# Optimization experiments

Hardware: AMD Instinct MI355X
Metric: run time of the kernel (lower is better)

## Reference

```python
import jax, jax.numpy as jnp
import numpy as np

N = 100000
E = 3200000
D = 128
H = 128
BN_EPS = 1e-5


def setup_inputs() -> dict:
    key = jax.random.key(0)
    ks = jax.random.split(key, 8)
    x = jax.random.normal(ks[0], (N, D), dtype=jnp.float32)
    edge_index = jax.random.randint(ks[1], (2, E), 0, N, dtype=jnp.int64)
    edge_attr = jax.random.normal(ks[2], (E, 1), dtype=jnp.float32)
    # MLP params (Linear stores weight [out,in]; we keep [in,out] for x @ W)
    W1 = jax.random.normal(ks[3], (D, H), dtype=jnp.float32) / np.sqrt(D)
    b1 = jnp.zeros((H,), dtype=jnp.float32)
    W2 = jax.random.normal(ks[4], (H, H), dtype=jnp.float32) / np.sqrt(H)
    b2 = jnp.zeros((H,), dtype=jnp.float32)
    gamma = jnp.ones((H,), dtype=jnp.float32)
    beta = jnp.zeros((H,), dtype=jnp.float32)
    return {"x": x, "edge_index": edge_index, "edge_attr": edge_attr,
            "W1": W1, "b1": b1, "W2": W2, "b2": b2,
            "gamma": gamma, "beta": beta}


def reference(x, edge_index, edge_attr, W1, b1, W2, b2, gamma, beta):
    src, dst = edge_index[0], edge_index[1]
    # GIN aggregation: (1 + eps) * x_i + sum_{j->i} x_j, eps = 0
    agg = jax.ops.segment_sum(x[src], dst, num_segments=N)  # [N, D]
    h = x + agg
    # 2-layer MLP
    h = jax.nn.relu(h @ W1 + b1)
    h = h @ W2 + b2
    # outer ReLU
    h = jax.nn.relu(h)
    # BatchNorm1d (training mode: batch stats, biased variance)
    mean = jnp.mean(h, axis=0)
    var = jnp.mean(jnp.square(h - mean), axis=0)
    h = (h - mean) * jax.lax.rsqrt(var + BN_EPS) * gamma + beta
    return h
```

## Files before the change

### kernel.cpp

```cpp
#include <hip/hip_runtime.h>

#define N_NODES 100000
#define DIM 128
#define NBUCK 391
#define CAP 12288
#define PT_TILE 8192
#define PT_THR 512

typedef unsigned int u32;
typedef unsigned short u16;
typedef __attribute__((ext_vector_type(8))) short bf16x8;
typedef __attribute__((ext_vector_type(4))) float f32x4;

__device__ __forceinline__ float bf16_to_f(u16 v) {
  return __uint_as_float(((u32)v) << 16);
}
__device__ __forceinline__ u16 f_to_bf16(float f) {
  u32 b = __float_as_uint(f);
  b += 0x7fff + ((b >> 16) & 1);
  return (u16)(b >> 16);
}
__device__ __forceinline__ float blo(u32 q) { return __uint_as_float(q << 16); }
__device__ __forceinline__ float bhi(u32 q) {
  return __uint_as_float(q & 0xffff0000u);
}
__device__ __forceinline__ u32 packbf(float lo, float hi) {
  return ((u32)f_to_bf16(hi) << 16) | (u32)f_to_bf16(lo);
}

__global__ __launch_bounds__(256) void prep_kernel(
    const float* __restrict__ x, u16* __restrict__ xb,
    const float* __restrict__ W1, u16* __restrict__ Wt1,
    const float* __restrict__ W2, u16* __restrict__ Wt2,
    const int* __restrict__ ei, int* __restrict__ bcnt, int E_) {
  int blk = blockIdx.x;
  if (blk < 2048) {
    int total = N_NODES * DIM / 4;
    int stride = 2048 * 256;
    for (int i = blk * 256 + threadIdx.x; i < total; i += stride) {
      float4 v = reinterpret_cast<const float4*>(x)[i];
      ushort4 o;
      o.x = f_to_bf16(v.x);
      o.y = f_to_bf16(v.y);
      o.z = f_to_bf16(v.z);
      o.w = f_to_bf16(v.w);
      reinterpret_cast<ushort4*>(xb)[i] = o;
    }
  } else if (blk < 2112) {
    int id = (blk - 2048) * 256 + threadIdx.x;
    Wt1[id] = f_to_bf16(W1[(id & 127) * DIM + (id >> 7)]);
  } else if (blk < 2176) {
    int id = (blk - 2112) * 256 + threadIdx.x;
    Wt2[id] = f_to_bf16(W2[(id & 127) * DIM + (id >> 7)]);
  } else {
    __shared__ int lc[NBUCK];
    for (int i = threadIdx.x; i < NBUCK; i += 256) lc[i] = 0;
    __syncthreads();
    const int* dst = ei + E_;
    int G = 512 * 256;
    int g = (blk - 2176) * 256 + threadIdx.x;
    int n4 = E_ >> 2;
    const int4* d4 = (const int4*)dst;
    for (int i = g; i < n4; i += G) {
      int4 v = d4[i];
      atomicAdd(&lc[((u32)v.x) >> 8], 1);
      atomicAdd(&lc[((u32)v.y) >> 8], 1);
      atomicAdd(&lc[((u32)v.z) >> 8], 1);
      atomicAdd(&lc[((u32)v.w) >> 8], 1);
    }
    for (int e = (n4 << 2) + g; e < E_; e += G)
      atomicAdd(&lc[((u32)dst[e]) >> 8], 1);
    __syncthreads();
    for (int i = threadIdx.x; i < NBUCK; i += 256)
      if (lc[i]) atomicAdd(&bcnt[i], lc[i]);
  }
}

__global__ void bscan_kernel(const int* __restrict__ bcnt,
                             int* __restrict__ boffs, int* __restrict__ gcur) {
  __shared__ int s[256];
  int t = threadIdx.x;
  int v0 = (2 * t < NBUCK) ? bcnt[2 * t] : 0;
  int v1 = (2 * t + 1 < NBUCK) ? bcnt[2 * t + 1] : 0;
  int ts = v0 + v1;
  s[t] = ts;
  __syncthreads();
  for (int o = 1; o < 256; o <<= 1) {
    int u = (t >= o) ? s[t - o] : 0;
    __syncthreads();
    s[t] += u;
    __syncthreads();
  }
  int excl = s[t] - ts;
  if (2 * t <= NBUCK) boffs[2 * t] = excl;
  if (2 * t + 1 <= NBUCK) boffs[2 * t + 1] = excl + v0;
  if (2 * t < NBUCK) gcur[2 * t] = excl;
  if (2 * t + 1 < NBUCK) gcur[2 * t + 1] = excl + v0;
}

__global__ __launch_bounds__(PT_THR) void partition_kernel(
    const int* __restrict__ ei, int* __restrict__ gcur,
    u32* __restrict__ packed, int E_) {
  __shared__ u32 keys[PT_TILE];
  __shared__ u16 bid[PT_TILE];
  __shared__ int lh[NBUCK];
  __shared__ int lpos[NBUCK];
  __shared__ int gpos[NBUCK];
  __shared__ int ss[PT_THR];
  const int t = threadIdx.x;
  const int base = blockIdx.x * PT_TILE;
  const int cnt = min(PT_TILE, E_ - base);

  for (int i = t; i < NBUCK; i += PT_THR) lh[i] = 0;
  __syncthreads();

  u32 pk[16];
  int bb[16];
#pragma unroll
  for (int k = 0; k < 16; ++k) {
    int e = base + k * PT_THR + t;
    if (k * PT_THR + t < cnt) {
      int src = ei[e];
      u32 dst = (u32)ei[E_ + e];
      bb[k] = (int)(dst >> 8);
      pk[k] = (u32)src | ((dst & 255u) << 17);
      atomicAdd(&lh[bb[k]], 1);
    } else {
      bb[k] = -1;
    }
  }
  __syncthreads();

  int v = (t < NBUCK) ? lh[t] : 0;
  ss[t] = v;
  __syncthreads();
  for (int o = 1; o < PT_THR; o <<= 1) {
    int u = (t >= o) ? ss[t - o] : 0;
    __syncthreads();
    ss[t] += u;
    __syncthreads();
  }
  if (t < NBUCK) {
    lpos[t] = ss[t] - v;
    if (v > 0) gpos[t] = atomicAdd(&gcur[t], v);
  }
  __syncthreads();

#pragma unroll
  for (int k = 0; k < 16; ++k) {
    if (bb[k] >= 0) {
      int p = atomicAdd(&lpos[bb[k]], 1);
      keys[p] = pk[k];
      bid[p] = (u16)bb[k];
    }
  }
  __syncthreads();

  for (int i = t; i < cnt; i += PT_THR) {
    int b = bid[i];
    int startb = lpos[b] - lh[b];
    packed[gpos[b] + (i - startb)] = keys[i];
  }
}

__global__ __launch_bounds__(256) void bsort_kernel(u32* __restrict__ packed,
                                                    const int* __restrict__ boffs,
                                                    int* __restrict__ offs,
                                                    int E_) {
  __shared__ u32 sorted_[CAP];
  __shared__ int hist[256], cur[256], ss[256];
  const int b = blockIdx.x, t = threadIdx.x;
  int base = boffs[b];
  int cnt = boffs[b + 1] - base;
  if (cnt > CAP) cnt = CAP;
  hist[t] = 0;
  __syncthreads();
  for (int i = t; i < cnt; i += 256) atomicAdd(&hist[packed[base + i] >> 17], 1);
  __syncthreads();
  int hv = hist[t];
  ss[t] = hv;
  __syncthreads();
  for (int o = 1; o < 256; o <<= 1) {
    int u = (t >= o) ? ss[t - o] : 0;
    __syncthreads();
    ss[t] += u;
    __syncthreads();
  }
  int excl = ss[t] - hv;
  cur[t] = excl;
  __syncthreads();
  for (int i = t; i < cnt; i += 256) {
    u32 v = packed[base + i];
    int p = atomicAdd(&cur[v >> 17], 1);
    sorted_[p] = v & 0x1FFFFu;
  }
  __syncthreads();
  for (int i = t; i < cnt; i += 256) packed[base + i] = sorted_[i];
  int node = b * 256 + t;
  if (node < N_NODES) offs[node] = base + excl;
  if (b == 0 && t == 0) offs[N_NODES] = E_;
}

__global__ __launch_bounds__(256) void gather_bf16_kernel(
    const uint4* __restrict__ xb4, const int* __restrict__ offs,
    const int* __restrict__ csr, uint4* __restrict__ hb4) {
  int n = blockIdx.x * 4 + (threadIdx.x >> 6);
  int lane = threadIdx.x & 63;
  int g = lane >> 4;
  int l = lane & 15;
  int beg = offs[n], end = offs[n + 1];
  float a0 = 0.f, a1 = 0.f, a2 = 0.f, a3 = 0.f;
  float a4 = 0.f, a5 = 0.f, a6 = 0.f, a7 = 0.f;
  if (g == 0) {
    uint4 q = xb4[(size_t)n * 16 + l];
    a0 = blo(q.x); a1 = bhi(q.x);
    a2 = blo(q.y); a3 = bhi(q.y);
    a4 = blo(q.z); a5 = bhi(q.z);
    a6 = blo(q.w); a7 = bhi(q.w);
  }
  int j = beg + g;
  for (; j + 12 < end; j += 16) {
    int s0 = csr[j], s1 = csr[j + 4], s2 = csr[j + 8], s3 = csr[j + 12];
    uint4 q0 = xb4[(size_t)s0 * 16 + l];
    uint4 q1 = xb4[(size_t)s1 * 16 + l];
    uint4 q2 = xb4[(size_t)s2 * 16 + l];
    uint4 q3 = xb4[(size_t)s3 * 16 + l];
    a0 += blo(q0.x); a1 += bhi(q0.x);
    a2 += blo(q0.y); a3 += bhi(q0.y);
    a4 += blo(q0.z); a5 += bhi(q0.z);
    a6 += blo(q0.w); a7 += bhi(q0.w);
    a0 += blo(q1.x); a1 += bhi(q1.x);
    a2 += blo(q1.y); a3 += bhi(q1.y);
    a4 += blo(q1.z); a5 += bhi(q1.z);
    a6 += blo(q1.w); a7 += bhi(q1.w);
    a0 += blo(q2.x); a1 += bhi(q2.x);
    a2 += blo(q2.y); a3 += bhi(q2.y);
    a4 += blo(q2.z); a5 += bhi(q2.z);
    a6 += blo(q2.w); a7 += bhi(q2.w);
    a0 += blo(q3.x); a1 += bhi(q3.x);
    a2 += blo(q3.y); a3 += bhi(q3.y);
    a4 += blo(q3.z); a5 += bhi(q3.z);
    a6 += blo(q3.w); a7 += bhi(q3.w);
  }
  for (; j < end; j += 4) {
    uint4 q = xb4[(size_t)csr[j] * 16 + l];
    a0 += blo(q.x); a1 += bhi(q.x);
    a2 += blo(q.y); a3 += bhi(q.y);
    a4 += blo(q.z); a5 += bhi(q.z);
    a6 += blo(q.w); a7 += bhi(q.w);
  }
  a0 += __shfl_xor(a0, 16); a1 += __shfl_xor(a1, 16);
  a2 += __shfl_xor(a2, 16); a3 += __shfl_xor(a3, 16);
  a4 += __shfl_xor(a4, 16); a5 += __shfl_xor(a5, 16);
  a6 += __shfl_xor(a6, 16); a7 += __shfl_xor(a7, 16);
  a0 += __shfl_xor(a0, 32); a1 += __shfl_xor(a1, 32);
  a2 += __shfl_xor(a2, 32); a3 += __shfl_xor(a3, 32);
  a4 += __shfl_xor(a4, 32); a5 += __shfl_xor(a5, 32);
  a6 += __shfl_xor(a6, 32); a7 += __shfl_xor(a7, 32);
  if (g == 0) {
    uint4 o;
    o.x = packbf(a0, a1);
    o.y = packbf(a2, a3);
    o.z = packbf(a4, a5);
    o.w = packbf(a6, a7);
    hb4[(size_t)n * 16 + l] = o;
  }
}

__global__ __launch_bounds__(256) void mlp_mfma_kernel(
    const u16* __restrict__ hb, const u16* __restrict__ Wt1,
    const u16* __restrict__ Wt2, const float* __restrict__ b1,
    const float* __restrict__ b2, float* __restrict__ out,
    float* __restrict__ pstats) {
  __shared__ u16 sH1[4][16 * DIM];
  __shared__ float sS[4][128], sQ[4][128];
  const int tid = threadIdx.x;
  const int wv = tid >> 6;
  const int lane = tid & 63;
  const int lr = lane & 15;
  const int lq = lane >> 4;
  const int row0 = blockIdx.x * 64 + wv * 16;

  bf16x8 a[4];
  {
    int r = row0 + lr;
    if (r > N_NODES - 1) r = N_NODES - 1;
#pragma unroll
    for (int ks = 0; ks < 4; ++ks)
      a[ks] = *reinterpret_cast<const bf16x8*>(hb + (size_t)r * DIM + ks * 32 +
                                               lq * 8);
  }
  f32x4 acc[8];
#pragma unroll
  for (int ct = 0; ct < 8; ++ct) {
    f32x4 c = {0.f, 0.f, 0.f, 0.f};
#pragma unroll
    for (int ks = 0; ks < 4; ++ks) {
      bf16x8 b = *reinterpret_cast<const bf16x8*>(
          Wt1 + (ct * 16 + lr) * DIM + ks * 32 + lq * 8);
      c = __builtin_amdgcn_mfma_f32_16x16x32_bf16(a[ks], b, c, 0, 0, 0);
    }
    acc[ct] = c;
  }
  char* slab = reinterpret_cast<char*>(&sH1[wv][0]);
#pragma unroll
  for (int ct = 0; ct < 8; ++ct) {
    int c = ct * 16 + lr;
    float bias = b1[c];
#pragma unroll
    for (int j = 0; j < 4; ++j) {
      int rl = lq * 4 + j;
      float y = fmaxf(acc[ct][j] + bias, 0.f);
      int byte = rl * 256 + ((c * 2) ^ ((rl & 7) << 4));
      *reinterpret_cast<u16*>(slab + byte) = f_to_bf16(y);
    }
  }
  __syncthreads();

  bf16x8 a2[4];
#pragma unroll
  for (int ks = 0; ks < 4; ++ks) {
    int byte = lr * 256 + (((ks * 32 + lq * 8) * 2) ^ ((lr & 7) << 4));
    a2[ks] = *reinterpret_cast<const bf16x8*>(slab + byte);
  }
#pragma unroll
  for (int ct = 0; ct < 8; ++ct) {
    f32x4 c = {0.f, 0.f, 0.f, 0.f};
#pragma unroll
    for (int ks = 0; ks < 4; ++ks) {
      bf16x8 b = *reinterpret_cast<const bf16x8*>(
          Wt2 + (ct * 16 + lr) * DIM + ks * 32 + lq * 8);
      c = __builtin_amdgcn_mfma_f32_16x16x32_bf16(a2[ks], b, c, 0, 0, 0);
    }
    acc[ct] = c;
  }
  float ls[8], lss[8];
#pragma unroll
  for (int ct = 0; ct < 8; ++ct) {
    int c = ct * 16 + lr;
    float bias = b2[c];
    ls[ct] = 0.f;
    lss[ct] = 0.f;
#pragma unroll
    for (int j = 0; j < 4; ++j) {
      int r = row0 + lq * 4 + j;
      float y = fmaxf(acc[ct][j] + bias, 0.f);
      if (r < N_NODES) {
        out[(size_t)r * DIM + c] = y;
        ls[ct] += y;
        lss[ct] += y * y;
      }
    }
  }
#pragma unroll
  for (int ct = 0; ct < 8; ++ct) {
    float s = ls[ct], q = lss[ct];
    s += __shfl_xor(s, 16);
    q += __shfl_xor(q, 16);
    s += __shfl_xor(s, 32);
    q += __shfl_xor(q, 32);
    if (lq == 0) {
      sS[wv][ct * 16 + lr] = s;
      sQ[wv][ct * 16 + lr] = q;
    }
  }
  __syncthreads();
  {
    int t = tid;
    float v;
    if (t < 128)
      v = sS[0][t] + sS[1][t] + sS[2][t] + sS[3][t];
    else
      v = sQ[0][t - 128] + sQ[1][t - 128] + sQ[2][t - 128] + sQ[3][t - 128];
    pstats[(size_t)blockIdx.x * 256 + t] = v;
  }
}

__global__ __launch_bounds__(256) void bn_reduce_kernel(
    const float* __restrict__ pstats, float* __restrict__ stats, int nblk) {
  int t = threadIdx.x;
  float v = 0.f;
  for (int i = blockIdx.x; i < nblk; i += gridDim.x)
    v += pstats[(size_t)i * 256 + t];
  atomicAdd(&stats[t], v);
}

__global__ void bn_scale_kernel(const float* __restrict__ stats,
                                const float* __restrict__ gamma,
                                const float* __restrict__ beta,
                                float* __restrict__ sc) {
  int c = threadIdx.x;
  float mean = stats[c] / (float)N_NODES;
  float var = stats[DIM + c] / (float)N_NODES - mean * mean;
  float scale = gamma[c] * rsqrtf(var + 1e-5f);
  sc[c] = scale;
  sc[DIM + c] = beta[c] - mean * scale;
}

__global__ __launch_bounds__(256) void bn_apply_kernel(
    float* __restrict__ h, const float* __restrict__ sc) {
  size_t total = (size_t)N_NODES * DIM / 4;
  size_t stride = (size_t)gridDim.x * blockDim.x;
  for (size_t i = (size_t)blockIdx.x * blockDim.x + threadIdx.x; i < total;
       i += stride) {
    float4 v = reinterpret_cast<float4*>(h)[i];
    int c = (int)((i * 4) & 127);
    v.x = v.x * sc[c + 0] + sc[DIM + c + 0];
    v.y = v.y * sc[c + 1] + sc[DIM + c + 1];
    v.z = v.z * sc[c + 2] + sc[DIM + c + 2];
    v.w = v.w * sc[c + 3] + sc[DIM + c + 3];
    reinterpret_cast<float4*>(h)[i] = v;
  }
}

__global__ __launch_bounds__(256) void hist_kernel(const int* __restrict__ ei,
                                                   int* __restrict__ deg,
                                                   int E_) {
  int stride = gridDim.x * blockDim.x;
  for (int e = blockIdx.x * blockDim.x + threadIdx.x; e < E_; e += stride)
    atomicAdd(&deg[ei[E_ + e]], 1);
}

__global__ __launch_bounds__(256) void scan_block_kernel(
    const int* __restrict__ deg, int* __restrict__ offs,
    int* __restrict__ partials, int n) {
  const int tid = threadIdx.x;
  int g = blockIdx.x * 1024 + tid * 4;
  int v0 = (g + 0 < n) ? deg[g + 0] : 0;
  int v1 = (g + 1 < n) ? deg[g + 1] : 0;
  int v2 = (g + 2 < n) ? deg[g + 2] : 0;
  int v3 = (g + 3 < n) ? deg[g + 3] : 0;
  int tsum = v0 + v1 + v2 + v3;
  __shared__ int s[256];
  s[tid] = tsum;
  __syncthreads();
  for (int off = 1; off < 256; off <<= 1) {
    int t = (tid >= off) ? s[tid - off] : 0;
    __syncthreads();
    s[tid] += t;
    __syncthreads();
  }
  int excl = s[tid] - tsum;
  if (g + 0 < n) offs[g + 0] = excl;
  if (g + 1 < n) offs[g + 1] = excl + v0;
  if (g + 2 < n) offs[g + 2] = excl + v0 + v1;
  if (g + 3 < n) offs[g + 3] = excl + v0 + v1 + v2;
  if (tid == 255) partials[blockIdx.x] = s[255];
}

__global__ void scan_partials_kernel(int* __restrict__ partials, int nb) {
  const int tid = threadIdx.x;
  int v = (tid < nb) ? partials[tid] : 0;
  __shared__ int s[128];
  s[tid] = v;
  __syncthreads();
  for (int off = 1; off < 128; off <<= 1) {
    int t = (tid >= off) ? s[tid - off] : 0;
    __syncthreads();
    s[tid] += t;
    __syncthreads();
  }
  if (tid < nb) partials[tid] = s[tid] - v;
}

__global__ __launch_bounds__(256) void scan_add_kernel(
    int* __restrict__ offs, int* __restrict__ cursor,
    const int* __restrict__ partials, int n, int E_) {
  int g = blockIdx.x * blockDim.x + threadIdx.x;
  if (g < n) {
    int v = offs[g] + partials[g >> 10];
    offs[g] = v;
    cursor[g] = v;
  }
  if (g == 0) offs[n] = E_;
}

__global__ __launch_bounds__(256) void fill_kernel(const int* __restrict__ ei,
                                                   int* __restrict__ cursor,
                                                   int* __restrict__ csr,
                                                   int E_) {
  const int G = gridDim.x * blockDim.x;
  int g = blockIdx.x * blockDim.x + threadIdx.x;
  for (long long base = g; base < E_; base += (long long)G * 8) {
    int src[8], dst[8], pos[8];
#pragma unroll
    for (int k = 0; k < 8; ++k) {
      long long e = base + (long long)k * G;
      src[k] = (e < E_) ? ei[e] : -1;
      dst[k] = (e < E_) ? ei[E_ + e] : 0;
    }
#pragma unroll
    for (int k = 0; k < 8; ++k)
      if (src[k] >= 0) pos[k] = atomicAdd(&cursor[dst[k]], 1);
#pragma unroll
    for (int k = 0; k < 8; ++k)
      if (src[k] >= 0) csr[pos[k]] = src[k];
  }
}

__global__ __launch_bounds__(128) void gather_f32_kernel(
    const float* __restrict__ x, const int* __restrict__ offs,
    const int* __restrict__ csr, float* __restrict__ h) {
  int n = blockIdx.x;
  int c = threadIdx.x;
  int beg = offs[n], end = offs[n + 1];
  float acc = x[(size_t)n * DIM + c];
  for (int j = beg; j < end; ++j) acc += x[(size_t)csr[j] * DIM + c];
  h[(size_t)n * DIM + c] = acc;
}

__global__ __launch_bounds__(256) void scatter_kernel(
    const float* __restrict__ x, const int* __restrict__ ei,
    float* __restrict__ h, int E_) {
  long long total = (long long)E_ * 32;
  long long stride = (long long)gridDim.x * blockDim.x;
  for (long long idx = (long long)blockIdx.x * blockDim.x + threadIdx.x;
       idx < total; idx += stride) {
    int e = (int)(idx >> 5);
    int q = (int)(idx & 31);
    float4 v =
        *reinterpret_cast<const float4*>(x + (size_t)ei[e] * DIM + q * 4);
    float* p = h + (size_t)ei[E_ + e] * DIM + q * 4;
    atomicAdd(p + 0, v.x);
    atomicAdd(p + 1, v.y);
    atomicAdd(p + 2, v.z);
    atomicAdd(p + 3, v.w);
  }
}

__global__ __launch_bounds__(256) void add_x_kernel(const float* __restrict__ x,
                                                    float* __restrict__ h) {
  size_t total = (size_t)N_NODES * DIM / 4;
  size_t stride = (size_t)gridDim.x * blockDim.x;
  for (size_t i = (size_t)blockIdx.x * blockDim.x + threadIdx.x; i < total;
       i += stride) {
    float4 v = reinterpret_cast<float4*>(h)[i];
    float4 xv = reinterpret_cast<const float4*>(x)[i];
    v.x += xv.x; v.y += xv.y; v.z += xv.z; v.w += xv.w;
    reinterpret_cast<float4*>(h)[i] = v;
  }
}

__global__ __launch_bounds__(256) void mlp_valu_kernel(
    float* hbuf, const float* __restrict__ W1, const float* __restrict__ b1,
    const float* __restrict__ W2, const float* __restrict__ b2) {
  __shared__ float sW[DIM * DIM];
  __shared__ float sH[32][DIM];
  const int tid = threadIdx.x;
  const int col = tid & 127;
  const int rhalf = tid >> 7;
  const int row0 = blockIdx.x * 32;

  for (int i = tid; i < DIM * DIM; i += 256) sW[i] = W1[i];
  for (int i = tid; i < 32 * DIM; i += 256) {
    int r = i >> 7, c = i & 127;
    sH[r][c] = hbuf[(size_t)(row0 + r) * DIM + c];
  }
  __syncthreads();
  float acc[16];
  float bias = b1[col];
#pragma unroll
  for (int j = 0; j < 16; ++j) acc[j] = bias;
#pragma unroll 4
  for (int k = 0; k < DIM; ++k) {
    float w = sW[k * DIM + col];
#pragma unroll
    for (int j = 0; j < 16; ++j) acc[j] = fmaf(sH[2 * j + rhalf][k], w, acc[j]);
  }
  __syncthreads();
  for (int i = tid; i < DIM * DIM; i += 256) sW[i] = W2[i];
#pragma unroll
  for (int j = 0; j < 16; ++j) sH[2 * j + rhalf][col] = fmaxf(acc[j], 0.f);
  __syncthreads();
  float bias2 = b2[col];
#pragma unroll
  for (int j = 0; j < 16; ++j) acc[j] = bias2;
#pragma unroll 4
  for (int k = 0; k < DIM; ++k) {
    float w = sW[k * DIM + col];
#pragma unroll
    for (int j = 0; j < 16; ++j) acc[j] = fmaf(sH[2 * j + rhalf][k], w, acc[j]);
  }
#pragma unroll
  for (int j = 0; j < 16; ++j)
    hbuf[(size_t)(row0 + 2 * j + rhalf) * DIM + col] = fmaxf(acc[j], 0.f);
}

__global__ __launch_bounds__(256) void bn_stats_kernel(
    const float* __restrict__ h, float* __restrict__ stats) {
  int col = threadIdx.x & 127;
  int rsub = threadIdx.x >> 7;
  int rstep = gridDim.x * 2;
  float s = 0.f, ss = 0.f;
  for (int r = blockIdx.x * 2 + rsub; r < N_NODES; r += rstep) {
    float v = h[(size_t)r * DIM + col];
    s += v;
    ss += v * v;
  }
  __shared__ float ls[256], lss[256];
  ls[threadIdx.x] = s;
  lss[threadIdx.x] = ss;
  __syncthreads();
  if (threadIdx.x < 128) {
    atomicAdd(&stats[col], ls[threadIdx.x] + ls[threadIdx.x + 128]);
    atomicAdd(&stats[DIM + col], lss[threadIdx.x] + lss[threadIdx.x + 128]);
  }
}

extern "C" void kernel_launch(void* const* d_in, const int* in_sizes, int n_in,
                              void* d_out, int out_size, void* d_ws,
                              size_t ws_size, hipStream_t stream) {
  const float* x = (const float*)d_in[0];
  const int* ei = (const int*)d_in[1];
  const float* W1 = (const float*)d_in[3];
  const float* b1 = (const float*)d_in[4];
  const float* W2 = (const float*)d_in[5];
  const float* b2 = (const float*)d_in[6];
  const float* gamma = (const float*)d_in[7];
  const float* beta = (const float*)d_in[8];
  float* out = (float*)d_out;
  int E_ = in_sizes[1] / 2;

  const size_t XB_B = (size_t)N_NODES * DIM * 2;
  char* w = (char*)d_ws;
  size_t off = 0;
  u16* xb = (u16*)(w + off); off += XB_B;
  u16* hb = (u16*)(w + off); off += XB_B;
  u16* Wt1 = (u16*)(w + off); off += 32768;
  u16* Wt2 = (u16*)(w + off); off += 32768;
  u32* packed = (u32*)(w + off); off += (size_t)E_ * 4;
  int* offs = (int*)(w + off); off += ((size_t)N_NODES + 4) * 4;
  int* bcnt = (int*)(w + off); off += 1600;
  float* stats = (float*)(w + off); off += 3072;
  int* boffs = (int*)(w + off); off += 1600;
  int* gcur = (int*)(w + off); off += 1600;
  size_t need_full = off;
  float* pstats = (float*)xb;

  int* f_offs = (int*)d_ws;
  int* f_cursor = f_offs + N_NODES + 1;
  int* f_partials = f_cursor + N_NODES;
  int* f_csr = f_partials + 128;
  float* f_stats = (float*)(f_csr + E_);
  size_t need_csr = ((size_t)2 * N_NODES + 129 + E_) * 4 + 3072;

  const int nScanBlocks = (N_NODES + 1023) / 1024;
  const int nEdgeBlocks = (E_ + 2047) / 2048;
  const int nPartBlocks = (E_ + PT_TILE - 1) / PT_TILE;
  const int nMlpBlocks = (N_NODES + 63) / 64;

  if (ws_size >= need_full) {
    hipMemsetAsync(bcnt, 0, 1600 + 3072, stream);
    prep_kernel<<<2688, 256, 0, stream>>>(x, xb, W1, Wt1, W2, Wt2, ei, bcnt,
                                          E_);
    bscan_kernel<<<1, 256, 0, stream>>>(bcnt, boffs, gcur);
    partition_kernel<<<nPartBlocks, PT_THR, 0, stream>>>(ei, gcur, packed, E_);
    bsort_kernel<<<NBUCK, 256, 0, stream>>>(packed, boffs, offs, E_);
    gather_bf16_kernel<<<N_NODES / 4, 256, 0, stream>>>(
        (const uint4*)xb, offs, (const int*)packed, (uint4*)hb);
    mlp_mfma_kernel<<<nMlpBlocks, 256, 0, stream>>>(hb, Wt1, Wt2, b1, b2, out,
                                                    pstats);
    bn_reduce_kernel<<<32, 256, 0, stream>>>(pstats, stats, nMlpBlocks);
    bn_scale_kernel<<<1, 128, 0, stream>>>(stats, gamma, beta, stats + 256);
    bn_apply_kernel<<<2048, 256, 0, stream>>>(out, stats + 256);
  } else if (ws_size >= need_csr) {
    hipMemsetAsync(f_cursor, 0, (size_t)N_NODES * sizeof(int), stream);
    hipMemsetAsync(f_stats, 0, 768 * sizeof(float), stream);
    hist_kernel<<<2048, 256, 0, stream>>>(ei, f_cursor, E_);
    scan_block_kernel<<<nScanBlocks, 256, 0, stream>>>(f_cursor, f_offs,
                                                       f_partials, N_NODES);
    scan_partials_kernel<<<1, 128, 0, stream>>>(f_partials, nScanBlocks);
    scan_add_kernel<<<(N_NODES + 255) / 256, 256, 0, stream>>>(
        f_offs, f_cursor, f_partials, N_NODES, E_);
    fill_kernel<<<nEdgeBlocks, 256, 0, stream>>>(ei, f_cursor, f_csr, E_);
    gather_f32_kernel<<<N_NODES, 128, 0, stream>>>(x, f_offs, f_csr, out);
    mlp_valu_kernel<<<(N_NODES + 31) / 32, 256, 0, stream>>>(out, W1, b1, W2,
                                                             b2);
    bn_stats_kernel<<<1024, 256, 0, stream>>>(out, f_stats);
    bn_scale_kernel<<<1, 128, 0, stream>>>(f_stats, gamma, beta, f_stats + 256);
    bn_apply_kernel<<<2048, 256, 0, stream>>>(out, f_stats + 256);
  } else {
    float* s2 = (float*)d_ws;
    hipMemsetAsync(out, 0, (size_t)N_NODES * DIM * sizeof(float), stream);
    hipMemsetAsync(s2, 0, 768 * sizeof(float), stream);
    scatter_kernel<<<4096, 256, 0, stream>>>(x, ei, out, E_);
    add_x_kernel<<<2048, 256, 0, stream>>>(x, out);
    mlp_valu_kernel<<<(N_NODES + 31) / 32, 256, 0, stream>>>(out, W1, b1, W2,
                                                             b2);
    bn_stats_kernel<<<1024, 256, 0, stream>>>(out, s2);
    bn_scale_kernel<<<1, 128, 0, stream>>>(s2, gamma, beta, s2 + 256);
    bn_apply_kernel<<<2048, 256, 0, stream>>>(out, s2 + 256);
  }
}
```

Baseline: 284.6 us.

## Store MLP output as bf16, fuse BN stats/apply, overlap x conversion with partition

The MLP kernel now writes its post-ReLU output as bf16 into the hb buffer instead of fp32 to out, and accumulates BN statistics with atomics straight into the stats array. This removes the reduce and scale kernels. A new apply kernel computes scale and shift per block and expands bf16 to the final fp32 output, which roughly halves the intermediate write and read traffic. The x-to-bf16 conversion moves from prep_kernel into extra blocks of the partition kernel so it runs alongside partitioning. The cost is an extra bf16 rounding of the output before normalisation, which adds precision error, and per-block atomics into 256 stat slots.

```diff
diff --git a/kernel.cpp b/kernel.cpp
--- a/kernel.cpp
+++ b/kernel.cpp
@@ -29,28 +29,15 @@
 }
 
 __global__ __launch_bounds__(256) void prep_kernel(
-    const float* __restrict__ x, u16* __restrict__ xb,
     const float* __restrict__ W1, u16* __restrict__ Wt1,
     const float* __restrict__ W2, u16* __restrict__ Wt2,
     const int* __restrict__ ei, int* __restrict__ bcnt, int E_) {
   int blk = blockIdx.x;
-  if (blk < 2048) {
-    int total = N_NODES * DIM / 4;
-    int stride = 2048 * 256;
-    for (int i = blk * 256 + threadIdx.x; i < total; i += stride) {
-      float4 v = reinterpret_cast<const float4*>(x)[i];
-      ushort4 o;
-      o.x = f_to_bf16(v.x);
-      o.y = f_to_bf16(v.y);
-      o.z = f_to_bf16(v.z);
-      o.w = f_to_bf16(v.w);
-      reinterpret_cast<ushort4*>(xb)[i] = o;
-    }
-  } else if (blk < 2112) {
-    int id = (blk - 2048) * 256 + threadIdx.x;
+  if (blk < 64) {
+    int id = blk * 256 + threadIdx.x;
     Wt1[id] = f_to_bf16(W1[(id & 127) * DIM + (id >> 7)]);
-  } else if (blk < 2176) {
-    int id = (blk - 2112) * 256 + threadIdx.x;
+  } else if (blk < 128) {
+    int id = (blk - 64) * 256 + threadIdx.x;
     Wt2[id] = f_to_bf16(W2[(id & 127) * DIM + (id >> 7)]);
   } else {
     __shared__ int lc[NBUCK];
@@ -58,7 +45,7 @@
     __syncthreads();
     const int* dst = ei + E_;
     int G = 512 * 256;
-    int g = (blk - 2176) * 256 + threadIdx.x;
+    int g = (blk - 128) * 256 + threadIdx.x;
     int n4 = E_ >> 2;
     const int4* d4 = (const int4*)dst;
     for (int i = g; i < n4; i += G) {
@@ -98,16 +85,35 @@
   if (2 * t + 1 < NBUCK) gcur[2 * t + 1] = excl + v0;
 }
 
-__global__ __launch_bounds__(PT_THR) void partition_kernel(
+__global__ __launch_bounds__(PT_THR) void part_cvt_kernel(
     const int* __restrict__ ei, int* __restrict__ gcur,
-    u32* __restrict__ packed, int E_) {
+    u32* __restrict__ packed, int E_, const float* __restrict__ x,
+    u16* __restrict__ xb) {
   __shared__ u32 keys[PT_TILE];
   __shared__ u16 bid[PT_TILE];
   __shared__ int lh[NBUCK];
   __shared__ int lpos[NBUCK];
   __shared__ int gpos[NBUCK];
   __shared__ int ss[PT_THR];
+  const int nPart = (E_ + PT_TILE - 1) / PT_TILE;
   const int t = threadIdx.x;
+
+  if (blockIdx.x >= nPart) {
+    int cb = blockIdx.x - nPart;
+    int total = N_NODES * DIM / 4;
+    int stride = 1024 * PT_THR;
+    for (int i = cb * PT_THR + t; i < total; i += stride) {
+      float4 v = reinterpret_cast<const float4*>(x)[i];
+      ushort4 o;
+      o.x = f_to_bf16(v.x);
+      o.y = f_to_bf16(v.y);
+      o.z = f_to_bf16(v.z);
+      o.w = f_to_bf16(v.w);
+      reinterpret_cast<ushort4*>(xb)[i] = o;
+    }
+    return;
+  }
+
   const int base = blockIdx.x * PT_TILE;
   const int cnt = min(PT_TILE, E_ - base);
 
@@ -268,10 +274,9 @@
 }
 
 __global__ __launch_bounds__(256) void mlp_mfma_kernel(
-    const u16* __restrict__ hb, const u16* __restrict__ Wt1,
+    u16* __restrict__ hb, const u16* __restrict__ Wt1,
     const u16* __restrict__ Wt2, const float* __restrict__ b1,
-    const float* __restrict__ b2, float* __restrict__ out,
-    float* __restrict__ pstats) {
+    const float* __restrict__ b2, float* __restrict__ stats) {
   __shared__ u16 sH1[4][16 * DIM];
   __shared__ float sS[4][128], sQ[4][128];
   const int tid = threadIdx.x;
@@ -345,10 +350,12 @@
     for (int j = 0; j < 4; ++j) {
       int r = row0 + lq * 4 + j;
       float y = fmaxf(acc[ct][j] + bias, 0.f);
+      u16 yq = f_to_bf16(y);
+      float yf = bf16_to_f(yq);
       if (r < N_NODES) {
-        out[(size_t)r * DIM + c] = y;
-        ls[ct] += y;
-        lss[ct] += y * y;
+        hb[(size_t)r * DIM + c] = yq;
+        ls[ct] += yf;
+        lss[ct] += yf * yf;
       }
     }
   }
@@ -372,44 +379,40 @@
       v = sS[0][t] + sS[1][t] + sS[2][t] + sS[3][t];
     else
       v = sQ[0][t - 128] + sQ[1][t - 128] + sQ[2][t - 128] + sQ[3][t - 128];
-    pstats[(size_t)blockIdx.x * 256 + t] = v;
-  }
-}
-
-__global__ __launch_bounds__(256) void bn_reduce_kernel(
-    const float* __restrict__ pstats, float* __restrict__ stats, int nblk) {
+    atomicAdd(&stats[t], v);
+  }
+}
+
+__global__ __launch_bounds__(256) void bn_apply_bf16_kernel(
+    const uint4* __restrict__ hb4, const float* __restrict__ stats,
+    const float* __restrict__ gamma, const float* __restrict__ beta,
+    float4* __restrict__ out4) {
+  __shared__ float sSc[128], sSh[128];
   int t = threadIdx.x;
-  float v = 0.f;
-  for (int i = blockIdx.x; i < nblk; i += gridDim.x)
-    v += pstats[(size_t)i * 256 + t];
-  atomicAdd(&stats[t], v);
-}
-
-__global__ void bn_scale_kernel(const float* __restrict__ stats,
-                                const float* __restrict__ gamma,
-                                const float* __restrict__ beta,
-                                float* __restrict__ sc) {
-  int c = threadIdx.x;
-  float mean = stats[c] / (float)N_NODES;
-  float var = stats[DIM + c] / (float)N_NODES - mean * mean;
-  float scale = gamma[c] * rsqrtf(var + 1e-5f);
-  sc[c] = scale;
-  sc[DIM + c] = beta[c] - mean * scale;
-}
-
-__global__ __launch_bounds__(256) void bn_apply_kernel(
-    float* __restrict__ h, const float* __restrict__ sc) {
-  size_t total = (size_t)N_NODES * DIM / 4;
-  size_t stride = (size_t)gridDim.x * blockDim.x;
-  for (size_t i = (size_t)blockIdx.x * blockDim.x + threadIdx.x; i < total;
-       i += stride) {
-    float4 v = reinterpret_cast<float4*>(h)[i];
-    int c = (int)((i * 4) & 127);
-    v.x = v.x * sc[c + 0] + sc[DIM + c + 0];
-    v.y = v.y * sc[c + 1] + sc[DIM + c + 1];
-    v.z = v.z * sc[c + 2] + sc[DIM + c + 2];
-    v.w = v.w * sc[c + 3] + sc[DIM + c + 3];
-    reinterpret_cast<float4*>(h)[i] = v;
+  if (t < 128) {
+    float mean = stats[t] / (float)N_NODES;
+    float var = stats[128 + t] / (float)N_NODES - mean * mean;
+    float scale = gamma[t] * rsqrtf(var + 1e-5f);
+    sSc[t] = scale;
+    sSh[t] = beta[t] - mean * scale;
+  }
+  __syncthreads();
+  int total = N_NODES * 16;
+  int stride = gridDim.x * 256;
+  for (int i = blockIdx.x * 256 + t; i < total; i += stride) {
+    uint4 q = hb4[i];
+    int cb = (i & 15) * 8;
+    float4 o0, o1;
+    o0.x = blo(q.x) * sSc[cb + 0] + sSh[cb + 0];
+    o0.y = bhi(q.x) * sSc[cb + 1] + sSh[cb + 1];
+    o0.z = blo(q.y) * sSc[cb + 2] + sSh[cb + 2];
+    o0.w = bhi(q.y) * sSc[cb + 3] + sSh[cb + 3];
+    o1.x = blo(q.z) * sSc[cb + 4] + sSh[cb + 4];
+    o1.y = bhi(q.z) * sSc[cb + 5] + sSh[cb + 5];
+    o1.z = blo(q.w) * sSc[cb + 6] + sSh[cb + 6];
+    o1.w = bhi(q.w) * sSc[cb + 7] + sSh[cb + 7];
+    out4[2 * i] = o0;
+    out4[2 * i + 1] = o1;
   }
 }
 
@@ -607,6 +610,34 @@
   }
 }
 
+__global__ void bn_scale_kernel(const float* __restrict__ stats,
+                                const float* __restrict__ gamma,
+                                const float* __restrict__ beta,
+                                float* __restrict__ sc) {
+  int c = threadIdx.x;
+  float mean = stats[c] / (float)N_NODES;
+  float var = stats[DIM + c] / (float)N_NODES - mean * mean;
+  float scale = gamma[c] * rsqrtf(var + 1e-5f);
+  sc[c] = scale;
+  sc[DIM + c] = beta[c] - mean * scale;
+}
+
+__global__ __launch_bounds__(256) void bn_apply_kernel(
+    float* __restrict__ h, const float* __restrict__ sc) {
+  size_t total = (size_t)N_NODES * DIM / 4;
+  size_t stride = (size_t)gridDim.x * blockDim.x;
+  for (size_t i = (size_t)blockIdx.x * blockDim.x + threadIdx.x; i < total;
+       i += stride) {
+    float4 v = reinterpret_cast<float4*>(h)[i];
+    int c = (int)((i * 4) & 127);
+    v.x = v.x * sc[c + 0] + sc[DIM + c + 0];
+    v.y = v.y * sc[c + 1] + sc[DIM + c + 1];
+    v.z = v.z * sc[c + 2] + sc[DIM + c + 2];
+    v.w = v.w * sc[c + 3] + sc[DIM + c + 3];
+    reinterpret_cast<float4*>(h)[i] = v;
+  }
+}
+
 extern "C" void kernel_launch(void* const* d_in, const int* in_sizes, int n_in,
                               void* d_out, int out_size, void* d_ws,
                               size_t ws_size, hipStream_t stream) {
@@ -635,7 +666,6 @@
   int* boffs = (int*)(w + off); off += 1600;
   int* gcur = (int*)(w + off); off += 1600;
   size_t need_full = off;
-  float* pstats = (float*)xb;
 
   int* f_offs = (int*)d_ws;
   int* f_cursor = f_offs + N_NODES + 1;
@@ -651,18 +681,17 @@
 
   if (ws_size >= need_full) {
     hipMemsetAsync(bcnt, 0, 1600 + 3072, stream);
-    prep_kernel<<<2688, 256, 0, stream>>>(x, xb, W1, Wt1, W2, Wt2, ei, bcnt,
-                                          E_);
+    prep_kernel<<<640, 256, 0, stream>>>(W1, Wt1, W2, Wt2, ei, bcnt, E_);
     bscan_kernel<<<1, 256, 0, stream>>>(bcnt, boffs, gcur);
-    partition_kernel<<<nPartBlocks, PT_THR, 0, stream>>>(ei, gcur, packed, E_);
+    part_cvt_kernel<<<nPartBlocks + 1024, PT_THR, 0, stream>>>(
+        ei, gcur, packed, E_, x, xb);
     bsort_kernel<<<NBUCK, 256, 0, stream>>>(packed, boffs, offs, E_);
     gather_bf16_kernel<<<N_NODES / 4, 256, 0, stream>>>(
         (const uint4*)xb, offs, (const int*)packed, (uint4*)hb);
-    mlp_mfma_kernel<<<nMlpBlocks, 256, 0, stream>>>(hb, Wt1, Wt2, b1, b2, out,
-                                                    pstats);
-    bn_reduce_kernel<<<32, 256, 0, stream>>>(pstats, stats, nMlpBlocks);
-    bn_scale_kernel<<<1, 128, 0, stream>>>(stats, gamma, beta, stats + 256);
-    bn_apply_kernel<<<2048, 256, 0, stream>>>(out, stats + 256);
+    mlp_mfma_kernel<<<nMlpBlocks, 256, 0, stream>>>(hb, Wt1, Wt2, b1, b2,
+                                                    stats);
+    bn_apply_bf16_kernel<<<2048, 256, 0, stream>>>(
+        (const uint4*)hb, stats, gamma, beta, (float4*)out);
   } else if (ws_size >= need_csr) {
     hipMemsetAsync(f_cursor, 0, (size_t)N_NODES * sizeof(int), stream);
     hipMemsetAsync(f_stats, 0, 768 * sizeof(float), stream);
```

Measured after the change: 289.3 us. No clear change (+1.7%).
